# Performance work log

Measured on AMD Instinct MI355X. Metric: run time of the kernel, lower is better.

Reference implementation:

```python
import jax, jax.numpy as jnp
import numpy as np

N_PATCHES = 7
HIDDEN = 256
HEADS = 8
BLOCKS = 4
OUT_D = 1000
BATCH = 256
C, H_IMG, W_IMG = 3, 224, 224
N_TOK = N_PATCHES ** 2 + 1  # 50 (CLS at node 0)
INPUT_D = C * (H_IMG // N_PATCHES) * (W_IMG // N_PATCHES)  # 3072
MLP_D = 4 * HIDDEN


def build_edge_index():
    # replicates get_squere_edge_index: 8-neighborhood grid (nodes shifted +1)
    # plus patch->CLS edges. Row 0 = source, row 1 = target (PyG convention).
    s, d = [], []
    for i in range(N_PATCHES):
        for j in range(N_PATCHES):
            a = i + j * N_PATCHES + 1
            for di, dj in [(-1, 0), (-1, -1), (0, -1), (1, -1), (1, 0), (1, 1), (0, 1), (-1, 1)]:
                ii, jj = i + di, j + dj
                if 0 <= ii < N_PATCHES and 0 <= jj < N_PATCHES:
                    s.append(a); d.append(ii + jj * N_PATCHES + 1)
    for i in range(N_PATCHES):
        for j in range(N_PATCHES):
            s.append(i + j * N_PATCHES + 1); d.append(0)
    return np.array([s, d], dtype=np.int64)


def pos_emb(S, d):
    i = jnp.arange(S, dtype=jnp.float32)[:, None]
    j = jnp.arange(d)
    jeff = (j // 2 * 2).astype(jnp.float32)
    ang = i / jnp.power(jnp.float32(10000.0), jeff / d)
    return jnp.where(j % 2 == 0, jnp.sin(ang), jnp.cos(ang))


def layer_norm(x, g, b):
    mu = x.mean(-1, keepdims=True)
    var = ((x - mu) ** 2).mean(-1, keepdims=True)
    return (x - mu) / jnp.sqrt(var + 1e-5) * g + b


def gat(x, src, dst, W, a_s, a_d, bias):
    # PyG GATConv: lin (no bias), per-head additive attention, LeakyReLU(0.2),
    # softmax over incoming edges per target, concat heads, + bias.
    B, N, _ = x.shape
    H, Dh = a_s.shape
    h = (x @ W).reshape(B, N, H, Dh)
    al_s = jnp.einsum('bnhd,hd->bnh', h, a_s)
    al_d = jnp.einsum('bnhd,hd->bnh', h, a_d)
    e = jax.nn.leaky_relu(al_s[:, src] + al_d[:, dst], 0.2)  # [B,E,H]
    seg_max = jax.vmap(lambda v: jax.ops.segment_max(v, dst, num_segments=N))
    seg_sum = jax.vmap(lambda v: jax.ops.segment_sum(v, dst, num_segments=N))
    m = jax.lax.stop_gradient(seg_max(e))
    ex = jnp.exp(e - m[:, dst])
    alpha = ex / (seg_sum(ex)[:, dst] + 1e-16)
    out = seg_sum(h[:, src] * alpha[..., None])  # [B,N,H,Dh]
    return out.reshape(B, N, H * Dh) + bias


def setup_inputs() -> dict:
    key = jax.random.key(0)
    ks = jax.random.split(key, 16)
    sc = 0.05
    L = BLOCKS
    inp = {
        'images': jax.random.normal(ks[0], (BATCH, C, H_IMG, W_IMG), jnp.float32),
        'edge_index': jnp.asarray(build_edge_index()),
        'Wmap': jax.random.normal(ks[1], (INPUT_D, HIDDEN), jnp.float32) * sc,
        'bmap': jax.random.normal(ks[2], (HIDDEN,), jnp.float32) * sc,
        'cls_tok': jax.random.uniform(ks[3], (1, HIDDEN), jnp.float32),
        'Wgat': jax.random.normal(ks[4], (L, HIDDEN, HIDDEN), jnp.float32) * sc,
        'att_src': jax.random.normal(ks[5], (L, HEADS, HIDDEN // HEADS), jnp.float32) * sc,
        'att_dst': jax.random.normal(ks[6], (L, HEADS, HIDDEN // HEADS), jnp.float32) * sc,
        'bgat': jax.random.normal(ks[7], (L, HIDDEN), jnp.float32) * sc,
        'ln1_g': jnp.ones((L, HIDDEN), jnp.float32),
        'ln1_b': jnp.zeros((L, HIDDEN), jnp.float32),
        'ln2_g': jnp.ones((L, HIDDEN), jnp.float32),
        'ln2_b': jnp.zeros((L, HIDDEN), jnp.float32),
        'W1': jax.random.normal(ks[8], (L, HIDDEN, MLP_D), jnp.float32) * sc,
        'b1': jax.random.normal(ks[9], (L, MLP_D), jnp.float32) * sc,
        'W2': jax.random.normal(ks[10], (L, MLP_D, HIDDEN), jnp.float32) * sc,
        'b2': jax.random.normal(ks[11], (L, HIDDEN), jnp.float32) * sc,
        'Wout': jax.random.normal(ks[12], (HIDDEN, OUT_D), jnp.float32) * sc,
        'bout': jax.random.normal(ks[13], (OUT_D,), jnp.float32) * sc,
    }
    return inp


def reference(images, edge_index, Wmap, bmap, cls_tok, Wgat, att_src, att_dst, bgat,
              ln1_g, ln1_b, ln2_g, ln2_b, W1, b1, W2, b2, Wout, bout):
    n, c, h, w = images.shape
    ps = h // N_PATCHES
    # vectorized patchify: [n, np^2, c*ps*ps] in (c, hh, ww) flatten order
    patches = images.reshape(n, c, N_PATCHES, ps, N_PATCHES, ps)
    patches = patches.transpose(0, 2, 4, 1, 3, 5).reshape(n, N_PATCHES ** 2, c * ps * ps)
    tok = patches @ Wmap + bmap
    tok = jnp.concatenate([jnp.broadcast_to(cls_tok, (n, 1, HIDDEN)), tok], axis=1)
    out = tok + pos_emb(N_TOK, HIDDEN)
    loops = jnp.arange(N_TOK)  # GATConv add_self_loops
    src = jnp.concatenate([edge_index[0], loops])
    dst = jnp.concatenate([edge_index[1], loops])
    for l in range(BLOCKS):
        out = out + gat(layer_norm(out, ln1_g[l], ln1_b[l]), src, dst,
                        Wgat[l], att_src[l], att_dst[l], bgat[l])
        h2 = layer_norm(out, ln2_g[l], ln2_b[l])
        out = out + (jax.nn.gelu(h2 @ W1[l] + b1[l], approximate=False) @ W2[l] + b2[l])
    return jax.nn.softmax(out[:, 0] @ Wout + bout, axis=-1)
```

## Files before the change

kernel.cpp:

```cpp
#include <hip/hip_runtime.h>
#include <hip/hip_bf16.h>

#define BATCH   256
#define NTOK    50
#define NPATCH  49
#define HID     256
#define HEADS   8
#define DH      32
#define NBLK    4
#define MLPD    1024
#define OUTD    1000
#define KPATCH  3072
#define MROWS   (BATCH*NTOK)
#define MPATCH  (BATCH*NPATCH)
#define MAXDEG  12

typedef __attribute__((ext_vector_type(4))) float  floatx4;
typedef __attribute__((ext_vector_type(8))) __bf16 bf16x8;
typedef __attribute__((ext_vector_type(4))) int    int4v;
typedef __attribute__((ext_vector_type(4))) short  short4v;

__device__ __forceinline__ bool tag_is_bf16(const unsigned short* tag) {
    return tag[0] == 0x3F80u;
}
__device__ __forceinline__ float ldf(const void* p, long i, bool bf) {
    return bf ? __bfloat162float(((const __hip_bfloat16*)p)[i])
              : ((const float*)p)[i];
}
__device__ __forceinline__ short bf16s(float x) {
    __hip_bfloat16 h = __float2bfloat16(x);
    return *(short*)&h;
}

__device__ __forceinline__ float fast_gelu(float u) {
    float s  = u * 0.70710678118654752f;
    float ax = fabsf(s);
    float t  = 1.f / (1.f + 0.3275911f * ax);
    float p  = fmaf(1.061405429f, t, -1.453152027f);
    p = fmaf(p, t, 1.421413741f);
    p = fmaf(p, t, -0.284496736f);
    p = fmaf(p, t, 0.254829592f);
    p *= t;
    float er = copysignf(1.f - p * __expf(-s * s), s);
    return 0.5f * u * (1.f + er);
}

#define OFF_BMAP 0
#define OFF_CLS  256
#define OFF_ASRC 512
#define OFF_ADST 1536
#define OFF_BGAT 2560
#define OFF_LN1G 3584
#define OFF_LN1B 4608
#define OFF_LN2G 5632
#define OFF_LN2B 6656
#define OFF_B1   7680
#define OFF_B2   11776
#define OFF_BOUT 12800
#define SP_TOTAL 13800

struct SmallSrc {
    const void *bmap, *cls, *asrc, *adst, *bgat, *ln1g, *ln1b, *ln2g, *ln2b, *b1, *b2, *bout;
};

__global__ void pack_params(SmallSrc s, const unsigned short* tag,
                            __hip_bfloat16* __restrict__ sp) {
    bool bf = tag_is_bf16(tag);
    int idx = blockIdx.x * 256 + threadIdx.x;
    if (idx >= SP_TOTAL) return;
    const void* src; long off;
    if      (idx < OFF_CLS)  { src = s.bmap; off = idx; }
    else if (idx < OFF_ASRC) { src = s.cls;  off = idx - OFF_CLS; }
    else if (idx < OFF_ADST) { src = s.asrc; off = idx - OFF_ASRC; }
    else if (idx < OFF_BGAT) { src = s.adst; off = idx - OFF_ADST; }
    else if (idx < OFF_LN1G) { src = s.bgat; off = idx - OFF_BGAT; }
    else if (idx < OFF_LN1B) { src = s.ln1g; off = idx - OFF_LN1G; }
    else if (idx < OFF_LN2G) { src = s.ln1b; off = idx - OFF_LN1B; }
    else if (idx < OFF_LN2B) { src = s.ln2g; off = idx - OFF_LN2G; }
    else if (idx < OFF_B1)   { src = s.ln2b; off = idx - OFF_LN2B; }
    else if (idx < OFF_B2)   { src = s.b1;   off = idx - OFF_B1; }
    else if (idx < OFF_BOUT) { src = s.b2;   off = idx - OFF_B2; }
    else                     { src = s.bout; off = idx - OFF_BOUT; }
    sp[idx] = __float2bfloat16(ldf(src, off, bf));
}

__global__ void prep_kernel(const int* __restrict__ ei, int E0,
                            float* __restrict__ adj, float* __restrict__ pe,
                            int* __restrict__ nbrI, float* __restrict__ nbrW,
                            int* __restrict__ deg) {
    int tid = threadIdx.x;
    if (blockIdx.x == 0) {
        for (int i = tid; i < NTOK * NTOK; i += 64) adj[i] = 0.f;
        __syncthreads();
        bool is64 = (ei[1] == 0);
        for (int e = tid; e < E0; e += 64) {
            int s, d;
            if (is64) { s = ei[2 * e]; d = ei[2 * (E0 + e)]; }
            else      { s = ei[e];     d = ei[E0 + e]; }
            if ((unsigned)s < NTOK && (unsigned)d < NTOK)
                atomicAdd(&adj[d * NTOK + s], 1.f);
        }
        if (tid < NTOK) atomicAdd(&adj[tid * NTOK + tid], 1.f);
        __syncthreads();
        if (tid > 0 && tid < NTOK) {
            int d = 0;
            for (int s = 0; s < NTOK; ++s) {
                float c = adj[tid * NTOK + s];
                if (c > 0.f && d < MAXDEG) { nbrI[tid * MAXDEG + d] = s;
                                             nbrW[tid * MAXDEG + d] = c; ++d; }
            }
            deg[tid] = d;
        }
        if (tid == 0) deg[0] = 0;
    } else {
        int t = blockIdx.x - 1;
        for (int j = tid; j < HID; j += 64) {
            float jeff = (float)(j & ~1);
            float ang = (float)t / powf(10000.f, jeff / (float)HID);
            pe[t * HID + j] = ((j & 1) == 0) ? sinf(ang) : cosf(ang);
        }
    }
}

__global__ __launch_bounds__(256) void transpose2(
    const void* __restrict__ Wmap, const void* __restrict__ Wgat,
    const void* __restrict__ W1,   const void* __restrict__ W2,
    const void* __restrict__ Wout, const unsigned short* tag,
    __hip_bfloat16* __restrict__ wmapT, __hip_bfloat16* __restrict__ wgatT,
    __hip_bfloat16* __restrict__ w1T,   __hip_bfloat16* __restrict__ w2T,
    __hip_bfloat16* __restrict__ woutT) {
    __shared__ __hip_bfloat16 tl[64][65];
    bool bf = tag_is_bf16(tag);
    int b = blockIdx.x;
    const void* src; __hip_bfloat16* dst; int R, C, tR; long so, dofs;
    if (b < 192)      { src = Wmap; dst = wmapT; R = 3072; C = 256;  tR = 48;
                        so = 0; dofs = 0; }
    else if (b < 256) { int ti = b - 192, l = ti >> 4; b = ti & 15;
                        src = Wgat; dst = wgatT; R = 256; C = 256; tR = 4;
                        so = (long)l * 65536; dofs = so; goto tiled; }
    else if (b < 512) { int ti = b - 256, l = ti >> 6; b = ti & 63;
                        src = W1; dst = w1T; R = 256; C = 1024; tR = 4;
                        so = (long)l * 262144; dofs = so; goto tiled; }
    else if (b < 768) { int ti = b - 512, l = ti >> 6; b = ti & 63;
                        src = W2; dst = w2T; R = 1024; C = 256; tR = 16;
                        so = (long)l * 262144; dofs = so; goto tiled; }
    else              { b -= 768; src = Wout; dst = woutT; R = 256; C = 1000;
                        tR = 4; so = 0; dofs = 0; }
tiled:
    int r0 = (b % tR) * 64, c0 = (b / tR) * 64;
    int tx = threadIdx.x & 63, ty = threadIdx.x >> 6;
#pragma unroll
    for (int j = 0; j < 16; ++j) {
        int rr = ty + 4 * j;
        float v = (c0 + tx < C) ? ldf(src, so + (long)(r0 + rr) * C + c0 + tx, bf) : 0.f;
        tl[rr][tx] = __float2bfloat16(v);
    }
    __syncthreads();
#pragma unroll
    for (int j = 0; j < 16; ++j) {
        int i2 = ty + 4 * j;
        if (c0 + i2 < C)
            dst[dofs + (long)(c0 + i2) * R + r0 + tx] = tl[tx][i2];
    }
}

__global__ void init_resid(const __hip_bfloat16* __restrict__ sp,
                           const float* __restrict__ pe, float* __restrict__ resid) {
    int idx = blockIdx.x * 256 + threadIdx.x;
    int row = idx >> 6, c4 = (idx & 63) * 4, t = row % NTOK;
    floatx4 o;
#pragma unroll
    for (int i = 0; i < 4; ++i) {
        int c = c4 + i;
        o[i] = (t == 0) ? __bfloat162float(sp[OFF_CLS + c]) + pe[c]
                        : __bfloat162float(sp[OFF_BMAP + c]) + pe[t * HID + c];
    }
    ((floatx4*)resid)[idx] = o;
}

__global__ __launch_bounds__(256) void patch_gemm64(
    const void* __restrict__ img, const __hip_bfloat16* __restrict__ wmapT,
    const unsigned short* tag, float* __restrict__ resid) {
    __shared__ short As[2][64][32];
    __shared__ short Bs[2][64][32];
    bool bf = tag_is_bf16(tag);
    int tid = threadIdx.x;
    int L = blockIdx.x;
    int w = (L & 7) * 98 + (L >> 3);
    int m0 = (w >> 2) * 64, n0 = (w & 3) * 64;
    int lr = tid >> 2, lc = (tid & 3) * 8;
    int lane = tid & 63, wave = tid >> 6;
    int wm = (wave >> 1) * 32, wn = (wave & 1) * 32;
    int q = lane >> 4, r = lane & 15, q8 = q * 8;
    int mA = m0 + lr;
    long baseA;
    { int pb = mA / 49, pp = mA % 49; baseA = (long)pb * 150528 + (pp / 7) * 7168 + (pp % 7) * 32; }
    const short* Bg = (const short*)wmapT;
    long b0 = (long)(n0 + lr) * KPATCH + lc;
    floatx4 acc[2][2];
#pragma unroll
    for (int i = 0; i < 2; ++i)
#pragma unroll
        for (int j = 0; j < 2; ++j) acc[i][j] = floatx4{0.f, 0.f, 0.f, 0.f};
    floatx4 f0_0, f1_0, f0_1, f1_1;
    bf16x8  h_0, h_1;
    int4v   bv_0, bv_1;
    auto loadA = [&](int ku, floatx4& f0, floatx4& f1, bf16x8& h) {
        long g = baseA + (ku >> 5) * 50176 + (ku & 31) * 224 + lc;
        if (bf) { h = *(const bf16x8*)(((const __bf16*)img) + g); }
        else    { const float* f = (const float*)img;
                  f0 = *(const floatx4*)(f + g);
                  f1 = *(const floatx4*)(f + g + 4); }
    };
    auto cvtA = [&](const floatx4& f0, const floatx4& f1, const bf16x8& h) -> bf16x8 {
        if (bf) return h;
        union { bf16x8 v; __hip_bfloat16 hh[8]; } u;
#pragma unroll
        for (int j = 0; j < 4; ++j) { u.hh[j]     = __float2bfloat16(f0[j]);
                                      u.hh[4 + j] = __float2bfloat16(f1[j]); }
        return u.v;
    };
    loadA(0, f0_0, f1_0, h_0); bv_0 = *(const int4v*)(Bg + b0);
    loadA(1, f0_1, f1_1, h_1); bv_1 = *(const int4v*)(Bg + b0 + 32);
    *(bf16x8*)&As[0][lr][lc] = cvtA(f0_0, f1_0, h_0);
    *(int4v*)&Bs[0][lr][lc]  = bv_0;
    loadA(2, f0_0, f1_0, h_0); bv_0 = *(const int4v*)(Bg + b0 + 64);
    __syncthreads();
    for (int kt = 0; kt < 96; kt += 2) {
        {
            *(bf16x8*)&As[1][lr][lc] = cvtA(f0_1, f1_1, h_1);
            *(int4v*)&Bs[1][lr][lc]  = bv_1;
            if (kt + 3 < 96) {
                loadA(kt + 3, f0_1, f1_1, h_1);
                bv_1 = *(const int4v*)(Bg + b0 + (long)(kt + 3) * 32);
            }
            bf16x8 af[2], bfv[2];
#pragma unroll
            for (int i = 0; i < 2; ++i) af[i]  = *(const bf16x8*)&As[0][wm + 16 * i + r][q8];
#pragma unroll
            for (int j = 0; j < 2; ++j) bfv[j] = *(const bf16x8*)&Bs[0][wn + 16 * j + r][q8];
#pragma unroll
            for (int i = 0; i < 2; ++i)
#pragma unroll
                for (int j = 0; j < 2; ++j)
                    acc[i][j] = __builtin_amdgcn_mfma_f32_16x16x32_bf16(af[i], bfv[j], acc[i][j], 0, 0, 0);
            __syncthreads();
        }
        {
            if (kt + 2 < 96) {
                *(bf16x8*)&As[0][lr][lc] = cvtA(f0_0, f1_0, h_0);
                *(int4v*)&Bs[0][lr][lc]  = bv_0;
                if (kt + 4 < 96) {
                    loadA(kt + 4, f0_0, f1_0, h_0);
                    bv_0 = *(const int4v*)(Bg + b0 + (long)(kt + 4) * 32);
                }
            }
            bf16x8 af[2], bfv[2];
#pragma unroll
            for (int i = 0; i < 2; ++i) af[i]  = *(const bf16x8*)&As[1][wm + 16 * i + r][q8];
#pragma unroll
            for (int j = 0; j < 2; ++j) bfv[j] = *(const bf16x8*)&Bs[1][wn + 16 * j + r][q8];
#pragma unroll
            for (int i = 0; i < 2; ++i)
#pragma unroll
                for (int j = 0; j < 2; ++j)
                    acc[i][j] = __builtin_amdgcn_mfma_f32_16x16x32_bf16(af[i], bfv[j], acc[i][j], 0, 0, 0);
            __syncthreads();
        }
    }
#pragma unroll
    for (int j = 0; j < 2; ++j) {
        int col = n0 + wn + 16 * j + r;
#pragma unroll
        for (int i = 0; i < 2; ++i) {
#pragma unroll
            for (int reg = 0; reg < 4; ++reg) {
                int row = m0 + wm + 16 * i + q * 4 + reg;
                int bb = row / 49, pp = row % 49;
                long oi = ((long)bb * NTOK + pp + 1) * HID + col;
                resid[oi] += acc[i][j][reg];
            }
        }
    }
}

__global__ __launch_bounds__(1024) void fused_layers(
    float* __restrict__ resid, const __hip_bfloat16* __restrict__ sp,
    const __hip_bfloat16* __restrict__ wgatT, const __hip_bfloat16* __restrict__ w1T,
    const __hip_bfloat16* __restrict__ w2T,
    const float* __restrict__ adj, const int* __restrict__ nbrI,
    const float* __restrict__ nbrW, const int* __restrict__ deg) {
    __shared__ __align__(16) char smem[141392];
    float (*resS)[HID]  = (float (*)[HID])(smem);
    short (*xbS)[264]   = (short (*)[264])(smem + 51200);
    float (*hS)[HID]    = (float (*)[HID])(smem + 84992);
    short (*midS)[264]  = (short (*)[264])(smem + 84992);
    float (*als)[HEADS] = (float (*)[HEADS])(smem + 51200);
    float (*ald)[HEADS] = (float (*)[HEADS])(smem + 52800);
    float (*alpha0)[NTOK] = (float (*)[NTOK])(smem + 54400);
    float (*alphaC)[NTOK][MAXDEG] = (float (*)[NTOK][MAXDEG])(smem + 56000);
    float* attS = (float*)(smem + 75200);
    float* attD = (float*)(smem + 76224);
    float* bgv  = (float*)(smem + 77248);
    int   (*nIs)[MAXDEG] = (int (*)[MAXDEG])(smem + 136192);
    float (*nWs)[MAXDEG] = (float (*)[MAXDEG])(smem + 138592);
    int*   dgs  = (int*)(smem + 140992);
    float* adj0 = (float*)(smem + 141192);

    int b = blockIdx.x, tid = threadIdx.x;
    int wave = tid >> 6, lane = tid & 63;
    int q = lane >> 4, r = lane & 15, q8 = q * 8;
    int nq = wave * 16;

    float* rg = resid + (long)b * (NTOK * HID);
    for (int i = tid; i < NTOK * HID / 4; i += 1024)
        ((floatx4*)resS)[i] = ((const floatx4*)rg)[i];
    for (int i = tid; i < 14 * 132; i += 1024) ((int*)&xbS[50][0])[i] = 0;
    if (tid < NTOK * MAXDEG) {
        ((int*)nIs)[tid] = nbrI[tid];
        ((float*)nWs)[tid] = nbrW[tid];
    }
    if (tid < NTOK) { dgs[tid] = deg[tid]; adj0[tid] = adj[tid]; }
    __syncthreads();

    for (int l = 0; l < NBLK; ++l) {
        {
            const __hip_bfloat16* gp = sp + OFF_LN1G + l * HID;
            const __hip_bfloat16* bp = sp + OFF_LN1B + l * HID;
            float gv[4], bvv[4];
#pragma unroll
            for (int u = 0; u < 4; ++u) { gv[u]  = __bfloat162float(gp[lane + 64 * u]);
                                          bvv[u] = __bfloat162float(bp[lane + 64 * u]); }
            for (int row = wave; row < NTOK; row += 16) {
                float v[4];
#pragma unroll
                for (int u = 0; u < 4; ++u) v[u] = resS[row][lane + 64 * u];
                float s = v[0] + v[1] + v[2] + v[3];
#pragma unroll
                for (int off = 32; off; off >>= 1) s += __shfl_xor(s, off, 64);
                float mu = s * (1.f / HID), d2 = 0.f;
#pragma unroll
                for (int u = 0; u < 4; ++u) { float d = v[u] - mu; d2 += d * d; }
#pragma unroll
                for (int off = 32; off; off >>= 1) d2 += __shfl_xor(d2, off, 64);
                float rstd = rsqrtf(d2 * (1.f / HID) + 1e-5f);
#pragma unroll
                for (int u = 0; u < 4; ++u)
                    xbS[row][lane + 64 * u] = bf16s((v[u] - mu) * rstd * gv[u] + bvv[u]);
            }
        }
        __syncthreads();
        {
            const short* Bg = (const short*)wgatT + (long)l * HID * HID;
            const short* Bp = Bg + (long)(nq + r) * HID + q8;
            bf16x8 bv[8];
#pragma unroll
            for (int kk = 0; kk < 8; ++kk) bv[kk] = *(const bf16x8*)(Bp + kk * 32);
            floatx4 acc[4];
#pragma unroll
            for (int i = 0; i < 4; ++i) acc[i] = floatx4{0.f, 0.f, 0.f, 0.f};
#pragma unroll
            for (int kk = 0; kk < 8; ++kk) {
#pragma unroll
                for (int i = 0; i < 4; ++i) {
                    bf16x8 af = *(const bf16x8*)&xbS[16 * i + r][kk * 32 + q8];
                    acc[i] = __builtin_amdgcn_mfma_f32_16x16x32_bf16(af, bv[kk], acc[i], 0, 0, 0);
                }
            }
            int col = nq + r;
#pragma unroll
            for (int i = 0; i < 4; ++i)
#pragma unroll
                for (int reg = 0; reg < 4; ++reg) {
                    int row = 16 * i + q * 4 + reg;
                    if (row < NTOK) hS[row][col] = acc[i][reg];
                }
        }
        __syncthreads();
        if (tid < HID) {
            attS[tid] = __bfloat162float(sp[OFF_ASRC + l * HID + tid]);
            attD[tid] = __bfloat162float(sp[OFF_ADST + l * HID + tid]);
            bgv[tid]  = __bfloat162float(sp[OFF_BGAT + l * HID + tid]);
        }
        __syncthreads();
        if (tid < NTOK * HEADS) {
            int s = tid >> 3, hh = tid & 7;
            float a1 = 0.f, a2 = 0.f;
#pragma unroll
            for (int d = 0; d < DH; ++d) {
                float hv = hS[s][hh * DH + d];
                a1 += hv * attS[hh * DH + d];
                a2 += hv * attD[hh * DH + d];
            }
            als[s][hh] = a1; ald[s][hh] = a2;
        }
        __syncthreads();
        if (tid < 512) {
            int hh = wave;
            int s = lane;
            float w = 0.f, e = -1e30f;
            if (s < NTOK) {
                w = adj0[s];
                if (w > 0.f) {
                    e = als[s][hh] + ald[0][hh];
                    e = (e > 0.f) ? e : 0.2f * e;
                }
            }
            float mx = e;
#pragma unroll
            for (int off = 32; off; off >>= 1) mx = fmaxf(mx, __shfl_xor(mx, off, 64));
            float v = (s < NTOK && w > 0.f) ? w * expf(e - mx) : 0.f;
            float sum = v;
#pragma unroll
            for (int off = 32; off; off >>= 1) sum += __shfl_xor(sum, off, 64);
            float inv = 1.f / (sum + 1e-16f);
            if (s < NTOK) alpha0[hh][s] = v * inv;
        } else {
            int t2 = tid - 512;
            if (t2 < NPATCH * HEADS) {
                int t = (t2 >> 3) + 1, hh = t2 & 7;
                float aldt = ald[t][hh];
                int d = dgs[t];
                float mx = -1e30f;
                for (int j = 0; j < d; ++j) {
                    float e = als[nIs[t][j]][hh] + aldt; e = (e > 0.f) ? e : 0.2f * e;
                    mx = fmaxf(mx, e);
                }
                float sum = 0.f;
                for (int j = 0; j < d; ++j) {
                    float e = als[nIs[t][j]][hh] + aldt; e = (e > 0.f) ? e : 0.2f * e;
                    float w = nWs[t][j] * expf(e - mx);
                    alphaC[hh][t][j] = w; sum += w;
                }
                float inv = 1.f / (sum + 1e-16f);
                for (int j = 0; j < d; ++j) alphaC[hh][t][j] *= inv;
            }
        }
        __syncthreads();
        {
            int quarter = tid >> 8;
            int col = tid & 255;
            int hd = col >> 5;
            float bgc = bgv[col];
            for (int t = quarter; t < NTOK; t += 4) {
                float a = 0.f;
                if (t == 0) {
                    for (int s = 0; s < NTOK; ++s) a += alpha0[hd][s] * hS[s][col];
                } else {
                    int d = dgs[t];
                    for (int j = 0; j < d; ++j) a += alphaC[hd][t][j] * hS[nIs[t][j]][col];
                }
                resS[t][col] += a + bgc;
            }
        }
        __syncthreads();
        {
            const __hip_bfloat16* gp = sp + OFF_LN2G + l * HID;
            const __hip_bfloat16* bp = sp + OFF_LN2B + l * HID;
            float gv[4], bvv[4];
#pragma unroll
            for (int u = 0; u < 4; ++u) { gv[u]  = __bfloat162float(gp[lane + 64 * u]);
                                          bvv[u] = __bfloat162float(bp[lane + 64 * u]); }
            for (int row = wave; row < NTOK; row += 16) {
                float v[4];
#pragma unroll
                for (int u = 0; u < 4; ++u) v[u] = resS[row][lane + 64 * u];
                float s = v[0] + v[1] + v[2] + v[3];
#pragma unroll
                for (int off = 32; off; off >>= 1) s += __shfl_xor(s, off, 64);
                float mu = s * (1.f / HID), d2 = 0.f;
#pragma unroll
                for (int u = 0; u < 4; ++u) { float d = v[u] - mu; d2 += d * d; }
#pragma unroll
                for (int off = 32; off; off >>= 1) d2 += __shfl_xor(d2, off, 64);
                float rstd = rsqrtf(d2 * (1.f / HID) + 1e-5f);
#pragma unroll
                for (int u = 0; u < 4; ++u)
                    xbS[row][lane + 64 * u] = bf16s((v[u] - mu) * rstd * gv[u] + bvv[u]);
            }
            for (int i = tid; i < 14 * 132; i += 1024) ((int*)&xbS[50][0])[i] = 0;
        }
        __syncthreads();
        {
            const short* Bg1 = (const short*)w1T + (long)l * HID * MLPD;
            const short* Bg2 = (const short*)w2T + (long)l * HID * MLPD;
            floatx4 acc2[4];
#pragma unroll
            for (int i = 0; i < 4; ++i) acc2[i] = floatx4{0.f, 0.f, 0.f, 0.f};
            for (int c = 0; c < 4; ++c) {
                {
                    const short* Bp = Bg1 + (long)(c * 256 + nq + r) * HID + q8;
                    bf16x8 bv[8];
#pragma unroll
                    for (int kk = 0; kk < 8; ++kk) bv[kk] = *(const bf16x8*)(Bp + kk * 32);
                    floatx4 accm[4];
#pragma unroll
                    for (int i = 0; i < 4; ++i) accm[i] = floatx4{0.f, 0.f, 0.f, 0.f};
#pragma unroll
                    for (int kk = 0; kk < 8; ++kk) {
#pragma unroll
                        for (int i = 0; i < 4; ++i) {
                            bf16x8 af = *(const bf16x8*)&xbS[16 * i + r][kk * 32 + q8];
                            accm[i] = __builtin_amdgcn_mfma_f32_16x16x32_bf16(af, bv[kk], accm[i], 0, 0, 0);
                        }
                    }
                    int colL = nq + r;
                    float b1v = __bfloat162float(sp[OFF_B1 + l * MLPD + c * 256 + colL]);
#pragma unroll
                    for (int i = 0; i < 4; ++i)
#pragma unroll
                        for (int reg = 0; reg < 4; ++reg) {
                            int row = 16 * i + q * 4 + reg;
                            midS[row][colL] = bf16s(fast_gelu(accm[i][reg] + b1v));
                        }
                }
                __syncthreads();
                {
                    const short* Bp = Bg2 + (long)(nq + r) * MLPD + c * 256 + q8;
                    bf16x8 bv[8];
#pragma unroll
                    for (int kk = 0; kk < 8; ++kk) bv[kk] = *(const bf16x8*)(Bp + kk * 32);
#pragma unroll
                    for (int kk = 0; kk < 8; ++kk) {
#pragma unroll
                        for (int i = 0; i < 4; ++i) {
                            bf16x8 af = *(const bf16x8*)&midS[16 * i + r][kk * 32 + q8];
                            acc2[i] = __builtin_amdgcn_mfma_f32_16x16x32_bf16(af, bv[kk], acc2[i], 0, 0, 0);
                        }
                    }
                }
                __syncthreads();
            }
            int col = nq + r;
            float b2v = __bfloat162float(sp[OFF_B2 + l * HID + col]);
#pragma unroll
            for (int i = 0; i < 4; ++i)
#pragma unroll
                for (int reg = 0; reg < 4; ++reg) {
                    int row = 16 * i + q * 4 + reg;
                    if (row < NTOK) resS[row][col] += acc2[i][reg] + b2v;
                }
        }
        __syncthreads();
    }
    for (int i = tid; i < NTOK * HID / 4; i += 1024)
        ((floatx4*)rg)[i] = ((const floatx4*)resS)[i];
}

__global__ __launch_bounds__(256) void head_gemm(
    const float* __restrict__ resid, const __hip_bfloat16* __restrict__ BT,
    const __hip_bfloat16* __restrict__ bias, float* __restrict__ logits, int N) {
    __shared__ short As[64][32];
    __shared__ short Bs[64][32];
    int tid = threadIdx.x;
    int m0 = blockIdx.x * 64, n0 = blockIdx.y * 64;
    int lr = tid >> 2, lc = (tid & 3) * 8;
    int lane = tid & 63, wave = tid >> 6;
    int wm = (wave >> 1) * 32, wn = (wave & 1) * 32;
    int q = lane >> 4, r = lane & 15, q8 = q * 8;
    const short* Bg = (const short*)BT;
    long a0 = (long)(m0 + lr) * (NTOK * HID) + lc;
    int bn = n0 + lr;
    long b0 = (long)bn * HID + lc;
    bool v0 = bn < N;
    floatx4 acc[2][2];
#pragma unroll
    for (int i = 0; i < 2; ++i)
#pragma unroll
        for (int j = 0; j < 2; ++j) acc[i][j] = floatx4{0.f, 0.f, 0.f, 0.f};
    int4v za = {0, 0, 0, 0};
    auto loadA = [&](int k0) -> bf16x8 {
        floatx4 f0 = *(const floatx4*)(resid + a0 + k0);
        floatx4 f1 = *(const floatx4*)(resid + a0 + k0 + 4);
        union { bf16x8 v; __hip_bfloat16 h[8]; } u;
#pragma unroll
        for (int i = 0; i < 4; ++i) { u.h[i] = __float2bfloat16(f0[i]);
                                      u.h[4 + i] = __float2bfloat16(f1[i]); }
        return u.v;
    };
    bf16x8 av = loadA(0);
    int4v bv = v0 ? *(const int4v*)(Bg + b0) : za;
    for (int kt = 0; kt < 8; ++kt) {
        __syncthreads();
        *(bf16x8*)&As[lr][lc] = av;
        *(int4v*)&Bs[lr][lc] = bv;
        __syncthreads();
        if (kt < 7) {
            av = loadA((kt + 1) * 32);
            bv = v0 ? *(const int4v*)(Bg + b0 + (kt + 1) * 32) : za;
        }
        bf16x8 af[2], bfv[2];
#pragma unroll
        for (int i = 0; i < 2; ++i) af[i]  = *(const bf16x8*)&As[wm + 16 * i + r][q8];
#pragma unroll
        for (int j = 0; j < 2; ++j) bfv[j] = *(const bf16x8*)&Bs[wn + 16 * j + r][q8];
#pragma unroll
        for (int i = 0; i < 2; ++i)
#pragma unroll
            for (int j = 0; j < 2; ++j)
                acc[i][j] = __builtin_amdgcn_mfma_f32_16x16x32_bf16(af[i], bfv[j], acc[i][j], 0, 0, 0);
    }
#pragma unroll
    for (int j = 0; j < 2; ++j) {
        int col = n0 + wn + 16 * j + r;
        if (col >= N) continue;
        float bvv = __bfloat162float(bias[col]);
#pragma unroll
        for (int i = 0; i < 2; ++i)
#pragma unroll
            for (int reg = 0; reg < 4; ++reg) {
                int row = m0 + wm + 16 * i + q * 4 + reg;
                logits[(long)row * N + col] = acc[i][j][reg] + bvv;
            }
    }
}

__global__ __launch_bounds__(256) void softmax_kernel(
    const float* __restrict__ logits, const unsigned short* tag, void* __restrict__ out) {
    __shared__ float red[8];
    bool bf = tag_is_bf16(tag);
    int b = blockIdx.x, tid = threadIdx.x;
    const float* Lr = logits + (long)b * OUTD;
    float v[4], mx = -1e30f;
#pragma unroll
    for (int i = 0; i < 4; ++i) {
        int j = tid + i * 256;
        v[i] = (j < OUTD) ? Lr[j] : -1e30f;
        mx = fmaxf(mx, v[i]);
    }
#pragma unroll
    for (int off = 32; off; off >>= 1) mx = fmaxf(mx, __shfl_xor(mx, off, 64));
    if ((tid & 63) == 0) red[tid >> 6] = mx;
    __syncthreads();
    mx = fmaxf(fmaxf(red[0], red[1]), fmaxf(red[2], red[3]));
    float s = 0.f, ex[4];
#pragma unroll
    for (int i = 0; i < 4; ++i) {
        int j = tid + i * 256;
        ex[i] = (j < OUTD) ? expf(v[i] - mx) : 0.f;
        s += ex[i];
    }
#pragma unroll
    for (int off = 32; off; off >>= 1) s += __shfl_xor(s, off, 64);
    __syncthreads();
    if ((tid & 63) == 0) red[4 + (tid >> 6)] = s;
    __syncthreads();
    float inv = 1.f / (red[4] + red[5] + red[6] + red[7]);
#pragma unroll
    for (int i = 0; i < 4; ++i) {
        int j = tid + i * 256;
        if (j < OUTD) {
            float o = ex[i] * inv;
            if (bf) ((__hip_bfloat16*)out)[(long)b * OUTD + j] = __float2bfloat16(o);
            else    ((float*)out)[(long)b * OUTD + j] = o;
        }
    }
}

extern "C" void kernel_launch(void* const* d_in, const int* in_sizes, int n_in,
                              void* d_out, int out_size, void* d_ws, size_t ws_size,
                              hipStream_t stream) {
    const void* images = d_in[0];
    const int*  ei     = (const int*)d_in[1];
    const unsigned short* tag = (const unsigned short*)d_in[9];
    int E0 = in_sizes[1] / 2;

    char* p = (char*)d_ws;
    auto alloc = [&](size_t bytes) { char* r = p; p += (bytes + 255) & ~(size_t)255; return r; };
    float*          resid  = (float*)alloc((size_t)MROWS * HID * 4);
    float*          logits = (float*)alloc((size_t)BATCH * OUTD * 4);
    float*          pe     = (float*)alloc((size_t)NTOK * HID * 4);
    float*          adj    = (float*)alloc((size_t)NTOK * NTOK * 4);
    int*            nbrI   = (int*)alloc((size_t)NTOK * MAXDEG * 4);
    float*          nbrW   = (float*)alloc((size_t)NTOK * MAXDEG * 4);
    int*            degp   = (int*)alloc((size_t)NTOK * 4);
    __hip_bfloat16* smallp = (__hip_bfloat16*)alloc((size_t)SP_TOTAL * 2);
    __hip_bfloat16* wmapT  = (__hip_bfloat16*)alloc((size_t)KPATCH * HID * 2);
    __hip_bfloat16* wgatT  = (__hip_bfloat16*)alloc((size_t)NBLK * HID * HID * 2);
    __hip_bfloat16* w1T    = (__hip_bfloat16*)alloc((size_t)NBLK * HID * MLPD * 2);
    __hip_bfloat16* w2T    = (__hip_bfloat16*)alloc((size_t)NBLK * HID * MLPD * 2);
    __hip_bfloat16* woutT  = (__hip_bfloat16*)alloc((size_t)HID * OUTD * 2);

    SmallSrc ss = { d_in[3], d_in[4], d_in[6], d_in[7], d_in[8], d_in[9], d_in[10],
                    d_in[11], d_in[12], d_in[14], d_in[16], d_in[18] };
    prep_kernel<<<51, 64, 0, stream>>>(ei, E0, adj, pe, nbrI, nbrW, degp);
    pack_params<<<(SP_TOTAL + 255) / 256, 256, 0, stream>>>(ss, tag, smallp);
    transpose2<<<832, 256, 0, stream>>>(d_in[2], d_in[5], d_in[13], d_in[15],
                                        d_in[17], tag, wmapT, wgatT, w1T, w2T, woutT);
    init_resid<<<MROWS * HID / 1024, 256, 0, stream>>>(smallp, pe, resid);
    patch_gemm64<<<784, 256, 0, stream>>>(images, wmapT, tag, resid);

    fused_layers<<<BATCH, 1024, 0, stream>>>(resid, smallp, wgatT, w1T, w2T,
                                             adj, nbrI, nbrW, degp);

    head_gemm<<<dim3(BATCH / 64, (OUTD + 63) / 64), 256, 0, stream>>>(
        resid, woutT, smallp + OFF_BOUT, logits, OUTD);
    softmax_kernel<<<BATCH, 256, 0, stream>>>(logits, tag, d_out);
}
```

Baseline: 629.3 us.

## Split-K patch GEMM into partial buffers, fold reduction into layer kernel, widen MLP chunks

The patch-embedding GEMM is split along K into two halves. This doubles the block count to 1568 so the GPU is better filled, and each half writes its partial sums to a separate buffer instead of doing a read-modify-write on resid. The fused layer kernel adds both partials while loading the residual into shared memory. The MLP inner loop now processes 512-column chunks in two passes instead of four 256-column passes, and shared arrays are padded to 260/520 strides to reduce bank conflicts. The cost is higher LDS usage (157KB) and extra global traffic for the partial buffers.

```diff
diff --git a/kernel.cpp b/kernel.cpp
--- a/kernel.cpp
+++ b/kernel.cpp
@@ -180,13 +180,15 @@
 
 __global__ __launch_bounds__(256) void patch_gemm64(
     const void* __restrict__ img, const __hip_bfloat16* __restrict__ wmapT,
-    const unsigned short* tag, float* __restrict__ resid) {
+    const unsigned short* tag, float* __restrict__ pbuf) {
     __shared__ short As[2][64][32];
     __shared__ short Bs[2][64][32];
     bool bf = tag_is_bf16(tag);
     int tid = threadIdx.x;
     int L = blockIdx.x;
-    int w = (L & 7) * 98 + (L >> 3);
+    int kc = L & 1;
+    int t = L >> 1;
+    int w = (t & 7) * 98 + (t >> 3);
     int m0 = (w >> 2) * 64, n0 = (w & 3) * 64;
     int lr = tid >> 2, lc = (tid & 3) * 8;
     int lane = tid & 63, wave = tid >> 6;
@@ -197,6 +199,7 @@
     { int pb = mA / 49, pp = mA % 49; baseA = (long)pb * 150528 + (pp / 7) * 7168 + (pp % 7) * 32; }
     const short* Bg = (const short*)wmapT;
     long b0 = (long)(n0 + lr) * KPATCH + lc;
+    int ku0 = kc * 48;
     floatx4 acc[2][2];
 #pragma unroll
     for (int i = 0; i < 2; ++i)
@@ -220,19 +223,19 @@
                                       u.hh[4 + j] = __float2bfloat16(f1[j]); }
         return u.v;
     };
-    loadA(0, f0_0, f1_0, h_0); bv_0 = *(const int4v*)(Bg + b0);
-    loadA(1, f0_1, f1_1, h_1); bv_1 = *(const int4v*)(Bg + b0 + 32);
+    loadA(ku0 + 0, f0_0, f1_0, h_0); bv_0 = *(const int4v*)(Bg + b0 + (long)ku0 * 32);
+    loadA(ku0 + 1, f0_1, f1_1, h_1); bv_1 = *(const int4v*)(Bg + b0 + (long)(ku0 + 1) * 32);
     *(bf16x8*)&As[0][lr][lc] = cvtA(f0_0, f1_0, h_0);
     *(int4v*)&Bs[0][lr][lc]  = bv_0;
-    loadA(2, f0_0, f1_0, h_0); bv_0 = *(const int4v*)(Bg + b0 + 64);
+    loadA(ku0 + 2, f0_0, f1_0, h_0); bv_0 = *(const int4v*)(Bg + b0 + (long)(ku0 + 2) * 32);
     __syncthreads();
-    for (int kt = 0; kt < 96; kt += 2) {
+    for (int kt = 0; kt < 48; kt += 2) {
         {
             *(bf16x8*)&As[1][lr][lc] = cvtA(f0_1, f1_1, h_1);
             *(int4v*)&Bs[1][lr][lc]  = bv_1;
-            if (kt + 3 < 96) {
-                loadA(kt + 3, f0_1, f1_1, h_1);
-                bv_1 = *(const int4v*)(Bg + b0 + (long)(kt + 3) * 32);
+            if (kt + 3 < 48) {
+                loadA(ku0 + kt + 3, f0_1, f1_1, h_1);
+                bv_1 = *(const int4v*)(Bg + b0 + (long)(ku0 + kt + 3) * 32);
             }
             bf16x8 af[2], bfv[2];
 #pragma unroll
@@ -247,12 +250,12 @@
             __syncthreads();
         }
         {
-            if (kt + 2 < 96) {
+            if (kt + 2 < 48) {
                 *(bf16x8*)&As[0][lr][lc] = cvtA(f0_0, f1_0, h_0);
                 *(int4v*)&Bs[0][lr][lc]  = bv_0;
-                if (kt + 4 < 96) {
-                    loadA(kt + 4, f0_0, f1_0, h_0);
-                    bv_0 = *(const int4v*)(Bg + b0 + (long)(kt + 4) * 32);
+                if (kt + 4 < 48) {
+                    loadA(ku0 + kt + 4, f0_0, f1_0, h_0);
+                    bv_0 = *(const int4v*)(Bg + b0 + (long)(ku0 + kt + 4) * 32);
                 }
             }
             bf16x8 af[2], bfv[2];
@@ -268,6 +271,7 @@
             __syncthreads();
         }
     }
+    long kofs = (long)kc * MPATCH * HID;
 #pragma unroll
     for (int j = 0; j < 2; ++j) {
         int col = n0 + wn + 16 * j + r;
@@ -276,36 +280,35 @@
 #pragma unroll
             for (int reg = 0; reg < 4; ++reg) {
                 int row = m0 + wm + 16 * i + q * 4 + reg;
-                int bb = row / 49, pp = row % 49;
-                long oi = ((long)bb * NTOK + pp + 1) * HID + col;
-                resid[oi] += acc[i][j][reg];
+                pbuf[kofs + (long)row * HID + col] = acc[i][j][reg];
             }
         }
     }
 }
 
 __global__ __launch_bounds__(1024) void fused_layers(
-    float* __restrict__ resid, const __hip_bfloat16* __restrict__ sp,
+    float* __restrict__ resid, const float* __restrict__ pbuf,
+    const __hip_bfloat16* __restrict__ sp,
     const __hip_bfloat16* __restrict__ wgatT, const __hip_bfloat16* __restrict__ w1T,
     const __hip_bfloat16* __restrict__ w2T,
     const float* __restrict__ adj, const int* __restrict__ nbrI,
     const float* __restrict__ nbrW, const int* __restrict__ deg) {
-    __shared__ __align__(16) char smem[141392];
-    float (*resS)[HID]  = (float (*)[HID])(smem);
-    short (*xbS)[264]   = (short (*)[264])(smem + 51200);
-    float (*hS)[HID]    = (float (*)[HID])(smem + 84992);
-    short (*midS)[264]  = (short (*)[264])(smem + 84992);
-    float (*als)[HEADS] = (float (*)[HEADS])(smem + 51200);
-    float (*ald)[HEADS] = (float (*)[HEADS])(smem + 52800);
-    float (*alpha0)[NTOK] = (float (*)[NTOK])(smem + 54400);
-    float (*alphaC)[NTOK][MAXDEG] = (float (*)[NTOK][MAXDEG])(smem + 56000);
-    float* attS = (float*)(smem + 75200);
-    float* attD = (float*)(smem + 76224);
-    float* bgv  = (float*)(smem + 77248);
-    int   (*nIs)[MAXDEG] = (int (*)[MAXDEG])(smem + 136192);
-    float (*nWs)[MAXDEG] = (float (*)[MAXDEG])(smem + 138592);
-    int*   dgs  = (int*)(smem + 140992);
-    float* adj0 = (float*)(smem + 141192);
+    __shared__ __align__(16) char smem[157552];
+    float (*resS)[260]  = (float (*)[260])(smem);
+    short (*xbS)[264]   = (short (*)[264])(smem + 52000);
+    float (*als)[HEADS] = (float (*)[HEADS])(smem + 52000);
+    float (*ald)[HEADS] = (float (*)[HEADS])(smem + 53600);
+    float (*alpha0)[NTOK] = (float (*)[NTOK])(smem + 55200);
+    float (*alphaC)[NTOK][MAXDEG] = (float (*)[NTOK][MAXDEG])(smem + 56800);
+    float* attS = (float*)(smem + 76000);
+    float* attD = (float*)(smem + 77024);
+    float* bgv  = (float*)(smem + 78048);
+    float (*hS)[260]    = (float (*)[260])(smem + 85792);
+    short (*midS)[520]  = (short (*)[520])(smem + 85792);
+    int   (*nIs)[MAXDEG] = (int (*)[MAXDEG])(smem + 152352);
+    float (*nWs)[MAXDEG] = (float (*)[MAXDEG])(smem + 154752);
+    int*   dgs  = (int*)(smem + 157152);
+    float* adj0 = (float*)(smem + 157352);
 
     int b = blockIdx.x, tid = threadIdx.x;
     int wave = tid >> 6, lane = tid & 63;
@@ -313,8 +316,18 @@
     int nq = wave * 16;
 
     float* rg = resid + (long)b * (NTOK * HID);
-    for (int i = tid; i < NTOK * HID / 4; i += 1024)
-        ((floatx4*)resS)[i] = ((const floatx4*)rg)[i];
+    const float* pA = pbuf;
+    const float* pB = pbuf + (long)MPATCH * HID;
+    for (int idx = tid; idx < NTOK * HID / 4; idx += 1024) {
+        int row = idx >> 6, c4 = (idx & 63) * 4;
+        floatx4 v = *(const floatx4*)(rg + (long)row * HID + c4);
+        if (row >= 1) {
+            long po = ((long)b * NPATCH + row - 1) * HID + c4;
+            v += *(const floatx4*)(pA + po);
+            v += *(const floatx4*)(pB + po);
+        }
+        *(floatx4*)&resS[row][c4] = v;
+    }
     for (int i = tid; i < 14 * 132; i += 1024) ((int*)&xbS[50][0])[i] = 0;
     if (tid < NTOK * MAXDEG) {
         ((int*)nIs)[tid] = nbrI[tid];
@@ -487,9 +500,11 @@
             floatx4 acc2[4];
 #pragma unroll
             for (int i = 0; i < 4; ++i) acc2[i] = floatx4{0.f, 0.f, 0.f, 0.f};
-            for (int c = 0; c < 4; ++c) {
-                {
-                    const short* Bp = Bg1 + (long)(c * 256 + nq + r) * HID + q8;
+            for (int c = 0; c < 2; ++c) {
+#pragma unroll
+                for (int jg = 0; jg < 2; ++jg) {
+                    int colL = wave * 32 + jg * 16 + r;
+                    const short* Bp = Bg1 + (long)(c * 512 + colL) * HID + q8;
                     bf16x8 bv[8];
 #pragma unroll
                     for (int kk = 0; kk < 8; ++kk) bv[kk] = *(const bf16x8*)(Bp + kk * 32);
@@ -504,8 +519,7 @@
                             accm[i] = __builtin_amdgcn_mfma_f32_16x16x32_bf16(af, bv[kk], accm[i], 0, 0, 0);
                         }
                     }
-                    int colL = nq + r;
-                    float b1v = __bfloat162float(sp[OFF_B1 + l * MLPD + c * 256 + colL]);
+                    float b1v = __bfloat162float(sp[OFF_B1 + l * MLPD + c * 512 + colL]);
 #pragma unroll
                     for (int i = 0; i < 4; ++i)
 #pragma unroll
@@ -515,8 +529,9 @@
                         }
                 }
                 __syncthreads();
-                {
-                    const short* Bp = Bg2 + (long)(nq + r) * MLPD + c * 256 + q8;
+#pragma unroll
+                for (int h = 0; h < 2; ++h) {
+                    const short* Bp = Bg2 + (long)(nq + r) * MLPD + c * 512 + h * 256 + q8;
                     bf16x8 bv[8];
 #pragma unroll
                     for (int kk = 0; kk < 8; ++kk) bv[kk] = *(const bf16x8*)(Bp + kk * 32);
@@ -524,7 +539,7 @@
                     for (int kk = 0; kk < 8; ++kk) {
 #pragma unroll
                         for (int i = 0; i < 4; ++i) {
-                            bf16x8 af = *(const bf16x8*)&midS[16 * i + r][kk * 32 + q8];
+                            bf16x8 af = *(const bf16x8*)&midS[16 * i + r][h * 256 + kk * 32 + q8];
                             acc2[i] = __builtin_amdgcn_mfma_f32_16x16x32_bf16(af, bv[kk], acc2[i], 0, 0, 0);
                         }
                     }
@@ -543,8 +558,10 @@
         }
         __syncthreads();
     }
-    for (int i = tid; i < NTOK * HID / 4; i += 1024)
-        ((floatx4*)rg)[i] = ((const floatx4*)resS)[i];
+    for (int idx = tid; idx < NTOK * HID / 4; idx += 1024) {
+        int row = idx >> 6, c4 = (idx & 63) * 4;
+        *(floatx4*)(rg + (long)row * HID + c4) = *(const floatx4*)&resS[row][c4];
+    }
 }
 
 __global__ __launch_bounds__(256) void head_gemm(
@@ -668,6 +685,7 @@
     char* p = (char*)d_ws;
     auto alloc = [&](size_t bytes) { char* r = p; p += (bytes + 255) & ~(size_t)255; return r; };
     float*          resid  = (float*)alloc((size_t)MROWS * HID * 4);
+    float*          pbuf   = (float*)alloc((size_t)2 * MPATCH * HID * 4);
     float*          logits = (float*)alloc((size_t)BATCH * OUTD * 4);
     float*          pe     = (float*)alloc((size_t)NTOK * HID * 4);
     float*          adj    = (float*)alloc((size_t)NTOK * NTOK * 4);
@@ -688,9 +706,9 @@
     transpose2<<<832, 256, 0, stream>>>(d_in[2], d_in[5], d_in[13], d_in[15],
                                         d_in[17], tag, wmapT, wgatT, w1T, w2T, woutT);
     init_resid<<<MROWS * HID / 1024, 256, 0, stream>>>(smallp, pe, resid);
-    patch_gemm64<<<784, 256, 0, stream>>>(images, wmapT, tag, resid);
-
-    fused_layers<<<BATCH, 1024, 0, stream>>>(resid, smallp, wgatT, w1T, w2T,
+    patch_gemm64<<<1568, 256, 0, stream>>>(images, wmapT, tag, pbuf);
+
+    fused_layers<<<BATCH, 1024, 0, stream>>>(resid, pbuf, smallp, wgatT, w1T, w2T,
                                              adj, nbrI, nbrW, degp);
 
     head_gemm<<<dim3(BATCH / 64, (OUTD + 63) / 64), 256, 0, stream>>>(
```

Result: no change. 621.5 us (-1.2%).
